# Kernel optimization log

Hardware: AMD Instinct MI355X
Metric: run time of the kernel (lower is better)

Reference implementation:

```python
import jax, jax.numpy as jnp
import numpy as np

B, L, D, NH, K, R = 2, 1024, 768, 12, 24, 768
HD = D // NH            # head_dim = 64
NFFT = 2048             # nearest power of two >= 2*L-1


def _spectral_filters():
    # Hankel matrix Z_{ij} = 2 / ((i+j)^3 - (i+j)), top-K eigvecs scaled by sigma^{1/4}
    e = np.arange(1, L + 1, dtype=np.float64)
    ipj = e[:, None] + e[None, :]
    Z = 2.0 / (ipj ** 3 - ipj)
    sigma, phi = np.linalg.eigh(Z)
    phi_k = phi[:, -K:] * (sigma[-K:] ** 0.25)
    return jnp.asarray(phi_k, dtype=jnp.float32)  # (L, K)


def setup_inputs() -> dict:
    key = jax.random.key(0)
    ks = jax.random.split(key, 16)
    s = 0.02
    lin = lambda k_, i, o: jax.random.normal(k_, (i, o), jnp.float32) * s
    return {
        "x": jax.random.normal(ks[0], (B, L, D), jnp.float32),
        "stu_filters": _spectral_filters(),
        "M_inputs": jax.random.normal(ks[1], (D, R), jnp.float32) * s,
        "M_filters": jax.random.normal(ks[2], (K, R), jnp.float32) * s,
        "wq_w": lin(ks[3], D, D), "wq_b": jnp.zeros((D,), jnp.float32),
        "wk_w": lin(ks[4], D, D), "wk_b": jnp.zeros((D,), jnp.float32),
        "wv_w": lin(ks[5], D, D), "wv_b": jnp.zeros((D,), jnp.float32),
        "wg_w": lin(ks[6], D, D), "wg_b": jnp.zeros((D,), jnp.float32),
        "wo_w": lin(ks[7], D, D), "wo_b": jnp.zeros((D,), jnp.float32),
    }


def _stu_features(x, stu_filters, M_inputs, M_filters):
    # tensordot STU path: project inputs and filters to rank R, then FFT causal conv
    u = x @ M_inputs                       # (B, L, R)
    phi = stu_filters @ M_filters          # (L, R)
    sgn = jnp.where(jnp.arange(L) % 2 == 0, 1.0, -1.0)[None, :, None]  # (1, L, 1)
    V = jnp.fft.rfft(phi, n=NFFT, axis=0)  # (NFFT//2+1, R)
    U = jnp.stack([u, u * sgn], axis=-1)   # (B, L, R, 2)
    Uf = jnp.fft.rfft(U, n=NFFT, axis=1)   # (B, NFFT//2+1, R, 2)
    conv = jnp.fft.irfft(V[None, :, :, None] * Uf, n=NFFT, axis=1)[:, :L]  # (B, L, R, 2)
    u_plus = conv[..., 0]
    u_minus = conv[..., 1] * sgn
    return u_plus + u_minus               # (B, L, R) with R == D


def reference(x, stu_filters, M_inputs, M_filters,
              wq_w, wq_b, wk_w, wk_b, wv_w, wv_b,
              wg_w, wg_b, wo_w, wo_b):
    x_tilde = _stu_features(x, stu_filters, M_inputs, M_filters)  # (B, L, D)

    heads = lambda y: y.reshape(B, L, NH, HD).transpose(0, 2, 1, 3)  # (B, H, L, h)
    q = heads(x @ wq_w + wq_b)
    k = heads(x @ wk_w + wk_b)
    v = heads(x @ wv_w + wv_b)

    # causal linear attention via cumulative outer-product state
    Z = jnp.einsum('bhtp,bhtn->bhtpn', v, k)     # (B, H, L, h, h)
    Hc = jnp.cumsum(Z, axis=2)
    Y = jnp.einsum('bhtp,bhtpn->bhtn', q, Hc)    # (B, H, L, h)
    y_attn = Y.transpose(0, 2, 1, 3).reshape(B, L, D)

    gate = jax.nn.sigmoid(x @ wg_w + wg_b)
    y = x_tilde + (y_attn - x_tilde) * gate
    return y @ wo_w + wo_b
```

## Files before the change

### kernel.cpp

```cpp
#include <hip/hip_runtime.h>
#include <math.h>

#define B_  2
#define L_  1024
#define D_  768
#define NH_ 12
#define HD_ 64
#define K_  24
#define R_  768
#define NC_ 16
#define CS_ 64

typedef __bf16 bf16x8 __attribute__((ext_vector_type(8)));
typedef float f32x4 __attribute__((ext_vector_type(4)));
typedef unsigned short u16x8 __attribute__((ext_vector_type(8)));

__device__ inline unsigned short f2bf(float f) {
    union { float f; unsigned u; } v; v.f = f;
    unsigned r = v.u + 0x7FFFu + ((v.u >> 16) & 1u);
    return (unsigned short)(r >> 16);
}

__device__ inline ushort4 pack4(const f32x4 v) {
    ushort4 r;
    r.x = f2bf(v[0]); r.y = f2bf(v[1]); r.z = f2bf(v[2]); r.w = f2bf(v[3]);
    return r;
}

#define GLD_LDS16(g, l)                                                     \
    __builtin_amdgcn_global_load_lds(                                       \
        (const __attribute__((address_space(1))) void*)(g),                 \
        (__attribute__((address_space(3))) void*)(l), 16, 0, 0)

__global__ __launch_bounds__(256) void k_prep(const float* __restrict__ w0,
                                              const float* __restrict__ w1,
                                              const float* __restrict__ w2,
                                              const float* __restrict__ w3,
                                              const float* __restrict__ w4,
                                              const float* __restrict__ w5,
                                              unsigned short* __restrict__ Wt,
                                              const float* __restrict__ x,
                                              unsigned short* __restrict__ xb,
                                              const float* __restrict__ F,
                                              const float* __restrict__ Mf,
                                              float* __restrict__ phi2) {
    const int bid = blockIdx.x;
    const int tid = threadIdx.x;
    if (bid < 864) {
        const int z = bid / 144, rem = bid % 144;
        const float* W;
        switch (z) {
            case 0: W = w0; break;
            case 1: W = w1; break;
            case 2: W = w2; break;
            case 3: W = w3; break;
            case 4: W = w4; break;
            default: W = w5; break;
        }
        unsigned short* o = Wt + (size_t)z * D_ * D_;
        __shared__ float t[64][65];
        const int n0 = (rem % 12) * 64, k0 = (rem / 12) * 64;
        const int c = tid & 63, rq = tid >> 6;
#pragma unroll
        for (int i = 0; i < 16; ++i)
            t[rq + i * 4][c] = W[(size_t)(k0 + rq + i * 4) * D_ + n0 + c];
        __syncthreads();
#pragma unroll
        for (int i = 0; i < 16; ++i)
            o[(size_t)(n0 + rq + i * 4) * D_ + k0 + c] = f2bf(t[c][rq + i * 4]);
    } else if (bid < 1632) {
        const int i8 = ((bid - 864) * 256 + tid) * 8;
        float4 f0 = *reinterpret_cast<const float4*>(x + i8);
        float4 f1 = *reinterpret_cast<const float4*>(x + i8 + 4);
        u16x8 p;
        p[0] = f2bf(f0.x); p[1] = f2bf(f0.y); p[2] = f2bf(f0.z); p[3] = f2bf(f0.w);
        p[4] = f2bf(f1.x); p[5] = f2bf(f1.y); p[6] = f2bf(f1.z); p[7] = f2bf(f1.w);
        *reinterpret_cast<u16x8*>(xb + i8) = p;
    } else {
        const int idx = (bid - 1632) * 256 + tid;
        const int r = idx % R_;
        const int j = idx / R_;
        float acc = 0.f;
#pragma unroll
        for (int kk = 0; kk < K_; ++kk)
            acc += F[j * K_ + kk] * Mf[kk * R_ + r];
        phi2[idx] = 2.f * acc;
    }
}

template <int FM, int FN>
__device__ __forceinline__ void gemm_core(const unsigned short* __restrict__ A,
                                          const unsigned short* __restrict__ Bt,
                                          const float* __restrict__ bias,
                                          int mode,
                                          float* __restrict__ cf,
                                          unsigned short* __restrict__ cbf,
                                          unsigned short* __restrict__ ct,
                                          int N, int Kd,
                                          int bm, int bn, int tid) {
    constexpr int BM = 2 * FM * 16;
    constexpr int BN = 2 * FN * 16;
    __shared__ unsigned short As[2][BM * 64];
    __shared__ unsigned short Bs[2][BN * 64];
    const int lane = tid & 63, wave = tid >> 6;
    const int wm = (wave >> 1) * (FM * 16), wn = (wave & 1) * (FN * 16);
    const int l15 = lane & 15, lg = lane >> 4;

    f32x4 acc[FM][FN] = {};

    auto stage = [&](int buf, int k0) {
#pragma unroll
        for (int q = 0; q < FM; ++q) {
            const int s = q * 256 + tid;
            GLD_LDS16(A + (size_t)(bm + (s >> 3)) * Kd + k0 + (s & 7) * 8,
                      &As[buf][s * 8]);
        }
#pragma unroll
        for (int q = 0; q < FN; ++q) {
            const int s = q * 256 + tid;
            GLD_LDS16(Bt + (size_t)(bn + (s >> 3)) * Kd + k0 + (s & 7) * 8,
                      &Bs[buf][s * 8]);
        }
    };

    stage(0, 0);
    __syncthreads();
    int cur = 0;
    const int nt = Kd / 64;
    for (int t = 0; t < nt; ++t) {
        if (t + 1 < nt) stage(cur ^ 1, (t + 1) * 64);
#pragma unroll
        for (int ks = 0; ks < 2; ++ks) {
            const int kb = ks * 32 + lg * 8;
            bf16x8 a[FM], b[FN];
#pragma unroll
            for (int f = 0; f < FM; ++f)
                a[f] = *reinterpret_cast<const bf16x8*>(
                    &As[cur][(wm + f * 16 + l15) * 64 + kb]);
#pragma unroll
            for (int f = 0; f < FN; ++f)
                b[f] = *reinterpret_cast<const bf16x8*>(
                    &Bs[cur][(wn + f * 16 + l15) * 64 + kb]);
#pragma unroll
            for (int fm = 0; fm < FM; ++fm)
#pragma unroll
                for (int fn = 0; fn < FN; ++fn)
                    acc[fm][fn] = __builtin_amdgcn_mfma_f32_16x16x32_bf16(
                        a[fm], b[fn], acc[fm][fn], 0, 0, 0);
        }
        __syncthreads();
        cur ^= 1;
    }

#pragma unroll
    for (int fm = 0; fm < FM; ++fm)
#pragma unroll
        for (int fn = 0; fn < FN; ++fn) {
            const int col = bn + wn + fn * 16 + l15;
            const float bv = bias ? bias[col] : 0.f;
            const int r0 = bm + wm + fm * 16 + lg * 4;
            f32x4 v = acc[fm][fn];
            v[0] += bv; v[1] += bv; v[2] += bv; v[3] += bv;
            if (mode == 0) {
#pragma unroll
                for (int j = 0; j < 4; ++j)
                    cf[(size_t)(r0 + j) * N + col] = v[j];
            }
            if (mode & 1) {
#pragma unroll
                for (int j = 0; j < 4; ++j)
                    cbf[(size_t)(r0 + j) * D_ + col] = f2bf(v[j]);
            }
            if (mode & 2) {
                const int h = col >> 6, n = col & 63;
                const int bI = r0 >> 10, l0 = r0 & 1023;
                *reinterpret_cast<ushort4*>(
                    ct + (((size_t)bI * NH_ + h) * 64 + n) * (size_t)L_ + l0) =
                    pack4(v);
            }
        }
}

__global__ __launch_bounds__(256) void k_gemm(const unsigned short* __restrict__ A,
                                              const unsigned short* __restrict__ Bt,
                                              const float* __restrict__ bias,
                                              float* __restrict__ C,
                                              int N, int Kd) {
    gemm_core<2, 2>(A, Bt, bias, 0, C, nullptr, nullptr, N, Kd,
                    blockIdx.y * 64, blockIdx.x * 64, threadIdx.x);
}

__global__ __launch_bounds__(256) void k_gemm5(const unsigned short* __restrict__ A,
                                               const unsigned short* __restrict__ wt,
                                               const float* __restrict__ bq,
                                               const float* __restrict__ bk,
                                               const float* __restrict__ bv,
                                               const float* __restrict__ bg,
                                               float* __restrict__ ubuf,
                                               unsigned short* __restrict__ qbf,
                                               unsigned short* __restrict__ ktb,
                                               unsigned short* __restrict__ vbf,
                                               unsigned short* __restrict__ vtb,
                                               float* __restrict__ gb) {
    const int z = blockIdx.z;
    const float* bias = nullptr;
    int mode = 0;
    float* cf = nullptr; unsigned short* cbf = nullptr; unsigned short* ct = nullptr;
    switch (z) {
        case 0: mode = 0; cf = ubuf; bias = nullptr; break;
        case 1: mode = 1; cbf = qbf; bias = bq; break;
        case 2: mode = 2; ct = ktb; bias = bk; break;
        case 3: mode = 3; cbf = vbf; ct = vtb; bias = bv; break;
        default: mode = 0; cf = gb; bias = bg; break;
    }
    const unsigned short* Bt = wt + (size_t)z * D_ * D_;
    gemm_core<4, 4>(A, Bt, bias, mode, cf, cbf, ct, D_, D_,
                    blockIdx.y * 128, blockIdx.x * 128, threadIdx.x);
}

__global__ __launch_bounds__(768) void k_conv(const float* __restrict__ u,
                                              const float* __restrict__ phi2,
                                              float* __restrict__ xt) {
    __shared__ f32x4 red[4][8][192];
    const int tid = threadIdx.x;
    const int g   = tid / 192;
    const int lr  = tid % 192;
    const int r   = lr * 4;
    const int m0  = blockIdx.x * 8;
    const int bp  = blockIdx.y;
    const int b   = bp >> 1, p = bp & 1;

    f32x4 acc[8] = {};
    f32x4 w[8]   = {};

    const int ns = g * 128;
    const int ne = min(ns + 128, m0 + 8);

    if (ns < ne) {
        if (g > 0) {
#pragma unroll
            for (int j = 1; j <= 7; ++j)
                w[(8 - j) & 7] =
                    *reinterpret_cast<const f32x4*>(phi2 + (size_t)(2 * (ns - j)) * R_ + r);
        }
        const float* pp = phi2 + (size_t)(2 * ns) * R_ + r;
        const float* up = u + ((size_t)(b * L_) + (size_t)(2 * (m0 + 7 - ns) + p)) * R_ + r;
        for (int i = ns; i < ne; i += 8) {
#pragma unroll
            for (int k = 0; k < 8; ++k) {
                const f32x4 wn = *reinterpret_cast<const f32x4*>(pp);
                const f32x4 un = *reinterpret_cast<const f32x4*>(up);
                w[k] = wn;
#pragma unroll
                for (int a = 0; a < 8; ++a)
                    acc[a] += w[(k + a + 1) & 7] * un;
                pp += 2 * R_;
                up -= 2 * R_;
            }
        }
    }

#pragma unroll
    for (int a = 0; a < 8; ++a) red[g][a][lr] = acc[a];
    __syncthreads();

#pragma unroll
    for (int q2 = 0; q2 < 2; ++q2) {
        const int sl = q2 * 768 + tid;
        const int a  = sl / 192, l = sl % 192;
        const f32x4 s = red[0][a][l] + red[1][a][l] + red[2][a][l] + red[3][a][l];
        *reinterpret_cast<f32x4*>(
            xt + ((size_t)(b * L_) + (size_t)(2 * (m0 + a) + p)) * R_ + l * 4) = s;
    }
}

__global__ __launch_bounds__(256) void k_attn(const unsigned short* __restrict__ qbf,
                                              const unsigned short* __restrict__ vbf,
                                              const unsigned short* __restrict__ ktb,
                                              const unsigned short* __restrict__ vtb,
                                              const float* __restrict__ xt,
                                              const float* __restrict__ g,
                                              unsigned short* __restrict__ gx) {
    const int c = blockIdx.x, h = blockIdx.y, b = blockIdx.z;
    __shared__ unsigned short Qs[64 * 64];
    __shared__ unsigned short Vs[64 * 64];
    __shared__ unsigned short Kc[64 * 64];
    __shared__ unsigned short Tk[64 * 64];
    __shared__ unsigned short Tv[64 * 64];
    __shared__ unsigned short Sl[64 * 72];
    __shared__ unsigned short Hl[64 * 72];

    const int tid = threadIdx.x;
    const int lane = tid & 63, wave = tid >> 6;
    const int wr = (wave >> 1) * 32, wc = (wave & 1) * 32;
    const int l15 = lane & 15, lg = lane >> 4;

    {
        const size_t rowbase = ((size_t)(b * L_ + c * CS_)) * D_ + h * HD_;
        const size_t tbase = ((size_t)(b * NH_ + h)) * 64 * (size_t)L_ + c * 64;
#pragma unroll
        for (int q2 = 0; q2 < 2; ++q2) {
            const int s = q2 * 256 + tid;
            const int row = s >> 3, c8 = s & 7;
            GLD_LDS16(qbf + rowbase + (size_t)row * D_ + c8 * 8, &Qs[s * 8]);
            GLD_LDS16(vbf + rowbase + (size_t)row * D_ + c8 * 8, &Vs[s * 8]);
            GLD_LDS16(ktb + tbase + (size_t)row * L_ + c8 * 8, &Kc[s * 8]);
        }
    }

    f32x4 hacc[2][2] = {};
    for (int cc = 0; cc < c; ++cc) {
        __syncthreads();
        const size_t tb2 = ((size_t)(b * NH_ + h)) * 64 * (size_t)L_ + cc * 64;
#pragma unroll
        for (int q2 = 0; q2 < 2; ++q2) {
            const int s = q2 * 256 + tid;
            const int row = s >> 3, c8 = s & 7;
            GLD_LDS16(ktb + tb2 + (size_t)row * L_ + c8 * 8, &Tk[s * 8]);
            GLD_LDS16(vtb + tb2 + (size_t)row * L_ + c8 * 8, &Tv[s * 8]);
        }
        __syncthreads();
#pragma unroll
        for (int ks = 0; ks < 2; ++ks) {
            const int kb = ks * 32 + lg * 8;
            bf16x8 av[2], bk[2];
#pragma unroll
            for (int f = 0; f < 2; ++f) {
                av[f] = *reinterpret_cast<const bf16x8*>(&Tv[(wr + f * 16 + l15) * 64 + kb]);
                bk[f] = *reinterpret_cast<const bf16x8*>(&Tk[(wc + f * 16 + l15) * 64 + kb]);
            }
#pragma unroll
            for (int fm = 0; fm < 2; ++fm)
#pragma unroll
                for (int fn = 0; fn < 2; ++fn)
                    hacc[fm][fn] = __builtin_amdgcn_mfma_f32_16x16x32_bf16(
                        av[fm], bk[fn], hacc[fm][fn], 0, 0, 0);
        }
    }
    __syncthreads();

    if (c > 0) {
#pragma unroll
        for (int fm = 0; fm < 2; ++fm)
#pragma unroll
            for (int fn = 0; fn < 2; ++fn) {
                const int n = wc + fn * 16 + l15;
                const int p0 = wr + fm * 16 + lg * 4;
                *reinterpret_cast<ushort4*>(&Hl[n * 72 + p0]) = pack4(hacc[fm][fn]);
            }
    }

    {
        f32x4 sacc[2][2] = {};
#pragma unroll
        for (int ks = 0; ks < 2; ++ks) {
            const int kb = ks * 32 + lg * 8;
            bf16x8 av[2], bq[2];
#pragma unroll
            for (int f = 0; f < 2; ++f) {
                av[f] = *reinterpret_cast<const bf16x8*>(&Vs[(wr + f * 16 + l15) * 64 + kb]);
                bq[f] = *reinterpret_cast<const bf16x8*>(&Qs[(wc + f * 16 + l15) * 64 + kb]);
            }
#pragma unroll
            for (int fm = 0; fm < 2; ++fm)
#pragma unroll
                for (int fn = 0; fn < 2; ++fn)
                    sacc[fm][fn] = __builtin_amdgcn_mfma_f32_16x16x32_bf16(
                        av[fm], bq[fn], sacc[fm][fn], 0, 0, 0);
        }
#pragma unroll
        for (int fm = 0; fm < 2; ++fm)
#pragma unroll
            for (int fn = 0; fn < 2; ++fn) {
                const int t = wc + fn * 16 + l15;
                const int s0 = wr + fm * 16 + lg * 4;
#pragma unroll
                for (int j = 0; j < 4; ++j)
                    if (s0 + j > t) sacc[fm][fn][j] = 0.f;
                *reinterpret_cast<ushort4*>(&Sl[t * 72 + s0]) = pack4(sacc[fm][fn]);
            }
    }
    __syncthreads();

    f32x4 yacc[2][2] = {};
#pragma unroll
    for (int ks = 0; ks < 2; ++ks) {
        const int kb = ks * 32 + lg * 8;
        bf16x8 ak[2], bs[2];
#pragma unroll
        for (int f = 0; f < 2; ++f) {
            ak[f] = *reinterpret_cast<const bf16x8*>(&Kc[(wr + f * 16 + l15) * 64 + kb]);
            bs[f] = *reinterpret_cast<const bf16x8*>(&Sl[(wc + f * 16 + l15) * 72 + kb]);
        }
#pragma unroll
        for (int fm = 0; fm < 2; ++fm)
#pragma unroll
            for (int fn = 0; fn < 2; ++fn)
                yacc[fm][fn] = __builtin_amdgcn_mfma_f32_16x16x32_bf16(
                    ak[fm], bs[fn], yacc[fm][fn], 0, 0, 0);
    }
    if (c > 0) {
#pragma unroll
        for (int ks = 0; ks < 2; ++ks) {
            const int kb = ks * 32 + lg * 8;
            bf16x8 ah[2], bq[2];
#pragma unroll
            for (int f = 0; f < 2; ++f) {
                ah[f] = *reinterpret_cast<const bf16x8*>(&Hl[(wr + f * 16 + l15) * 72 + kb]);
                bq[f] = *reinterpret_cast<const bf16x8*>(&Qs[(wc + f * 16 + l15) * 64 + kb]);
            }
#pragma unroll
            for (int fm = 0; fm < 2; ++fm)
#pragma unroll
                for (int fn = 0; fn < 2; ++fn)
                    yacc[fm][fn] = __builtin_amdgcn_mfma_f32_16x16x32_bf16(
                        ah[fm], bq[fn], yacc[fm][fn], 0, 0, 0);
        }
    }

#pragma unroll
    for (int fm = 0; fm < 2; ++fm)
#pragma unroll
        for (int fn = 0; fn < 2; ++fn) {
            const int n0 = wr + fm * 16 + lg * 4;
            const int t = wc + fn * 16 + l15;
            const size_t idx = ((size_t)(b * L_ + c * CS_ + t)) * D_ + h * HD_ + n0;
            const float4 gv = *reinterpret_cast<const float4*>(g + idx);
            const float4 xv = *reinterpret_cast<const float4*>(xt + idx);
            f32x4 y = yacc[fm][fn];
            ushort4 o;
            {
                const float s0 = 1.f / (1.f + expf(-gv.x));
                o.x = f2bf(xv.x + (y[0] - xv.x) * s0);
                const float s1 = 1.f / (1.f + expf(-gv.y));
                o.y = f2bf(xv.y + (y[1] - xv.y) * s1);
                const float s2 = 1.f / (1.f + expf(-gv.z));
                o.z = f2bf(xv.z + (y[2] - xv.z) * s2);
                const float s3 = 1.f / (1.f + expf(-gv.w));
                o.w = f2bf(xv.w + (y[3] - xv.w) * s3);
            }
            *reinterpret_cast<ushort4*>(gx + idx) = o;
        }
}

extern "C" void kernel_launch(void* const* d_in, const int* in_sizes, int n_in,
                              void* d_out, int out_size, void* d_ws, size_t ws_size,
                              hipStream_t stream) {
    const float* x    = (const float*)d_in[0];
    const float* stu  = (const float*)d_in[1];
    const float* Mi   = (const float*)d_in[2];
    const float* Mf   = (const float*)d_in[3];
    const float* wq_w = (const float*)d_in[4];
    const float* wq_b = (const float*)d_in[5];
    const float* wk_w = (const float*)d_in[6];
    const float* wk_b = (const float*)d_in[7];
    const float* wv_w = (const float*)d_in[8];
    const float* wv_b = (const float*)d_in[9];
    const float* wg_w = (const float*)d_in[10];
    const float* wg_b = (const float*)d_in[11];
    const float* wo_w = (const float*)d_in[12];
    const float* wo_b = (const float*)d_in[13];
    float* out = (float*)d_out;

    char* ws = (char*)d_ws;
    size_t o = 0;
    const size_t WSZ = (size_t)D_ * D_;
    unsigned short* wbf = (unsigned short*)(ws + o); o += 6 * WSZ * 2;
    unsigned short* xbf = (unsigned short*)(ws + o); o += (size_t)B_ * L_ * D_ * 2;
    unsigned short* gx  = (unsigned short*)(ws + o); o += (size_t)B_ * L_ * D_ * 2;
    unsigned short* qbf = (unsigned short*)(ws + o); o += (size_t)B_ * L_ * D_ * 2;
    unsigned short* vbf = (unsigned short*)(ws + o); o += (size_t)B_ * L_ * D_ * 2;
    unsigned short* ktb = (unsigned short*)(ws + o); o += (size_t)B_ * NH_ * 64 * L_ * 2;
    unsigned short* vtb = (unsigned short*)(ws + o); o += (size_t)B_ * NH_ * 64 * L_ * 2;
    float* ubuf = (float*)(ws + o); o += (size_t)B_ * L_ * R_ * 4;
    float* phi2 = (float*)(ws + o); o += (size_t)L_ * R_ * 4;
    float* xt   = (float*)(ws + o); o += (size_t)B_ * L_ * R_ * 4;
    float* gb   = (float*)(ws + o); o += (size_t)B_ * L_ * D_ * 4;

    unsigned short* wo_t = wbf + 5 * WSZ;

    const dim3 blk(256);

    k_prep<<<dim3(4704), blk, 0, stream>>>(Mi, wq_w, wk_w, wv_w, wg_w, wo_w, wbf,
                                           x, xbf, stu, Mf, phi2);

    k_gemm5<<<dim3(D_ / 128, (B_ * L_) / 128, 5), blk, 0, stream>>>(
        xbf, wbf, wq_b, wk_b, wv_b, wg_b, ubuf, qbf, ktb, vbf, vtb, gb);

    k_conv<<<dim3(L_ / 2 / 8, B_ * 2), dim3(768), 0, stream>>>(ubuf, phi2, xt);

    k_attn<<<dim3(NC_, NH_, B_), blk, 0, stream>>>(qbf, vbf, ktb, vtb, xt, gb, gx);

    k_gemm<<<dim3(D_ / 64, (B_ * L_) / 64), blk, 0, stream>>>(gx, wo_t, wo_b, out, D_, D_);
}
```

Before: 100.0 us.

## Store conv operands in bf16, compute only even filter taps, move gating into conv

The u and gate projections and the filter table are now stored as bf16 instead of fp32. Only the even-index filter rows are precomputed, since the conv only ever reads those, which halves the phi table and shrinks the prep grid. The gating blend moves from the attention kernel into the convolution kernel, which now runs after attention and reads a bf16 attention output. The conv reduction uses 8 groups of 64 taps with 8-wide vectors, and its cross-group partial sums are stored in bf16 in LDS, which risks extra precision loss in both operands and accumulation.

```diff
diff --git a/kernel.cpp b/kernel.cpp
--- a/kernel.cpp
+++ b/kernel.cpp
@@ -13,6 +13,7 @@
 
 typedef __bf16 bf16x8 __attribute__((ext_vector_type(8)));
 typedef float f32x4 __attribute__((ext_vector_type(4)));
+typedef float f32x8 __attribute__((ext_vector_type(8)));
 typedef unsigned short u16x8 __attribute__((ext_vector_type(8)));
 
 __device__ inline unsigned short f2bf(float f) {
@@ -24,6 +25,24 @@
 __device__ inline ushort4 pack4(const f32x4 v) {
     ushort4 r;
     r.x = f2bf(v[0]); r.y = f2bf(v[1]); r.z = f2bf(v[2]); r.w = f2bf(v[3]);
+    return r;
+}
+
+__device__ inline u16x8 pack8(const f32x8 v) {
+    u16x8 r;
+#pragma unroll
+    for (int e = 0; e < 8; ++e) r[e] = f2bf(v[e]);
+    return r;
+}
+
+__device__ inline f32x8 bf2f8(const u16x8 v) {
+    f32x8 r;
+#pragma unroll
+    for (int e = 0; e < 8; ++e) {
+        union { float f; unsigned u; } t;
+        t.u = ((unsigned)v[e]) << 16;
+        r[e] = t.f;
+    }
     return r;
 }
 
@@ -43,7 +62,7 @@
                                               unsigned short* __restrict__ xb,
                                               const float* __restrict__ F,
                                               const float* __restrict__ Mf,
-                                              float* __restrict__ phi2) {
+                                              unsigned short* __restrict__ phiev) {
     const int bid = blockIdx.x;
     const int tid = threadIdx.x;
     if (bid < 864) {
@@ -79,12 +98,12 @@
     } else {
         const int idx = (bid - 1632) * 256 + tid;
         const int r = idx % R_;
-        const int j = idx / R_;
+        const int n = idx / R_;
         float acc = 0.f;
 #pragma unroll
         for (int kk = 0; kk < K_; ++kk)
-            acc += F[j * K_ + kk] * Mf[kk * R_ + r];
-        phi2[idx] = 2.f * acc;
+            acc += F[(2 * n) * K_ + kk] * Mf[kk * R_ + r];
+        phiev[idx] = f2bf(2.f * acc);
     }
 }
 
@@ -196,91 +215,33 @@
                                                const float* __restrict__ bk,
                                                const float* __restrict__ bv,
                                                const float* __restrict__ bg,
-                                               float* __restrict__ ubuf,
+                                               unsigned short* __restrict__ ubf,
                                                unsigned short* __restrict__ qbf,
                                                unsigned short* __restrict__ ktb,
                                                unsigned short* __restrict__ vbf,
                                                unsigned short* __restrict__ vtb,
-                                               float* __restrict__ gb) {
+                                               unsigned short* __restrict__ gbf) {
     const int z = blockIdx.z;
     const float* bias = nullptr;
-    int mode = 0;
-    float* cf = nullptr; unsigned short* cbf = nullptr; unsigned short* ct = nullptr;
+    int mode = 1;
+    unsigned short* cbf = nullptr; unsigned short* ct = nullptr;
     switch (z) {
-        case 0: mode = 0; cf = ubuf; bias = nullptr; break;
+        case 0: mode = 1; cbf = ubf; bias = nullptr; break;
         case 1: mode = 1; cbf = qbf; bias = bq; break;
         case 2: mode = 2; ct = ktb; bias = bk; break;
         case 3: mode = 3; cbf = vbf; ct = vtb; bias = bv; break;
-        default: mode = 0; cf = gb; bias = bg; break;
+        default: mode = 1; cbf = gbf; bias = bg; break;
     }
     const unsigned short* Bt = wt + (size_t)z * D_ * D_;
-    gemm_core<4, 4>(A, Bt, bias, mode, cf, cbf, ct, D_, D_,
+    gemm_core<4, 4>(A, Bt, bias, mode, nullptr, cbf, ct, D_, D_,
                     blockIdx.y * 128, blockIdx.x * 128, threadIdx.x);
-}
-
-__global__ __launch_bounds__(768) void k_conv(const float* __restrict__ u,
-                                              const float* __restrict__ phi2,
-                                              float* __restrict__ xt) {
-    __shared__ f32x4 red[4][8][192];
-    const int tid = threadIdx.x;
-    const int g   = tid / 192;
-    const int lr  = tid % 192;
-    const int r   = lr * 4;
-    const int m0  = blockIdx.x * 8;
-    const int bp  = blockIdx.y;
-    const int b   = bp >> 1, p = bp & 1;
-
-    f32x4 acc[8] = {};
-    f32x4 w[8]   = {};
-
-    const int ns = g * 128;
-    const int ne = min(ns + 128, m0 + 8);
-
-    if (ns < ne) {
-        if (g > 0) {
-#pragma unroll
-            for (int j = 1; j <= 7; ++j)
-                w[(8 - j) & 7] =
-                    *reinterpret_cast<const f32x4*>(phi2 + (size_t)(2 * (ns - j)) * R_ + r);
-        }
-        const float* pp = phi2 + (size_t)(2 * ns) * R_ + r;
-        const float* up = u + ((size_t)(b * L_) + (size_t)(2 * (m0 + 7 - ns) + p)) * R_ + r;
-        for (int i = ns; i < ne; i += 8) {
-#pragma unroll
-            for (int k = 0; k < 8; ++k) {
-                const f32x4 wn = *reinterpret_cast<const f32x4*>(pp);
-                const f32x4 un = *reinterpret_cast<const f32x4*>(up);
-                w[k] = wn;
-#pragma unroll
-                for (int a = 0; a < 8; ++a)
-                    acc[a] += w[(k + a + 1) & 7] * un;
-                pp += 2 * R_;
-                up -= 2 * R_;
-            }
-        }
-    }
-
-#pragma unroll
-    for (int a = 0; a < 8; ++a) red[g][a][lr] = acc[a];
-    __syncthreads();
-
-#pragma unroll
-    for (int q2 = 0; q2 < 2; ++q2) {
-        const int sl = q2 * 768 + tid;
-        const int a  = sl / 192, l = sl % 192;
-        const f32x4 s = red[0][a][l] + red[1][a][l] + red[2][a][l] + red[3][a][l];
-        *reinterpret_cast<f32x4*>(
-            xt + ((size_t)(b * L_) + (size_t)(2 * (m0 + a) + p)) * R_ + l * 4) = s;
-    }
 }
 
 __global__ __launch_bounds__(256) void k_attn(const unsigned short* __restrict__ qbf,
                                               const unsigned short* __restrict__ vbf,
                                               const unsigned short* __restrict__ ktb,
                                               const unsigned short* __restrict__ vtb,
-                                              const float* __restrict__ xt,
-                                              const float* __restrict__ g,
-                                              unsigned short* __restrict__ gx) {
+                                              unsigned short* __restrict__ yab) {
     const int c = blockIdx.x, h = blockIdx.y, b = blockIdx.z;
     __shared__ unsigned short Qs[64 * 64];
     __shared__ unsigned short Vs[64 * 64];
@@ -425,22 +386,75 @@
             const int n0 = wr + fm * 16 + lg * 4;
             const int t = wc + fn * 16 + l15;
             const size_t idx = ((size_t)(b * L_ + c * CS_ + t)) * D_ + h * HD_ + n0;
-            const float4 gv = *reinterpret_cast<const float4*>(g + idx);
-            const float4 xv = *reinterpret_cast<const float4*>(xt + idx);
-            f32x4 y = yacc[fm][fn];
-            ushort4 o;
-            {
-                const float s0 = 1.f / (1.f + expf(-gv.x));
-                o.x = f2bf(xv.x + (y[0] - xv.x) * s0);
-                const float s1 = 1.f / (1.f + expf(-gv.y));
-                o.y = f2bf(xv.y + (y[1] - xv.y) * s1);
-                const float s2 = 1.f / (1.f + expf(-gv.z));
-                o.z = f2bf(xv.z + (y[2] - xv.z) * s2);
-                const float s3 = 1.f / (1.f + expf(-gv.w));
-                o.w = f2bf(xv.w + (y[3] - xv.w) * s3);
-            }
-            *reinterpret_cast<ushort4*>(gx + idx) = o;
-        }
+            *reinterpret_cast<ushort4*>(yab + idx) = pack4(yacc[fm][fn]);
+        }
+}
+
+__global__ __launch_bounds__(768) void k_conv(const unsigned short* __restrict__ ubf,
+                                              const unsigned short* __restrict__ phiev,
+                                              const unsigned short* __restrict__ yab,
+                                              const unsigned short* __restrict__ gbf,
+                                              unsigned short* __restrict__ gx) {
+    __shared__ u16x8 red[8][8][96];
+    const int tid = threadIdx.x;
+    const int g   = tid / 96;
+    const int lr  = tid % 96;
+    const int r   = lr * 8;
+    const int m0  = blockIdx.x * 8;
+    const int bp  = blockIdx.y;
+    const int b   = bp >> 1, p = bp & 1;
+
+    f32x8 acc[8] = {};
+    f32x8 w[8]   = {};
+
+    const int ns = g * 64;
+    const int ne = min(ns + 64, m0 + 8);
+
+    if (ns < ne) {
+        if (g > 0) {
+#pragma unroll
+            for (int j = 1; j <= 7; ++j)
+                w[(8 - j) & 7] = bf2f8(
+                    *reinterpret_cast<const u16x8*>(phiev + (size_t)(ns - j) * R_ + r));
+        }
+        const unsigned short* pp = phiev + (size_t)ns * R_ + r;
+        const unsigned short* up =
+            ubf + ((size_t)(b * L_) + (size_t)(2 * (m0 + 7 - ns) + p)) * R_ + r;
+        for (int i = ns; i < ne; i += 8) {
+#pragma unroll
+            for (int k = 0; k < 8; ++k) {
+                const u16x8 pv = *reinterpret_cast<const u16x8*>(pp);
+                const u16x8 uv = *reinterpret_cast<const u16x8*>(up);
+                w[k] = bf2f8(pv);
+                const f32x8 fu = bf2f8(uv);
+#pragma unroll
+                for (int a = 0; a < 8; ++a)
+                    acc[a] += w[(k + a + 1) & 7] * fu;
+                pp += R_;
+                up -= 2 * R_;
+            }
+        }
+    }
+
+#pragma unroll
+    for (int a = 0; a < 8; ++a) red[g][a][lr] = pack8(acc[a]);
+    __syncthreads();
+
+    const int a2 = tid / 96, l2 = tid % 96;
+    f32x8 s = {};
+#pragma unroll
+    for (int g2 = 0; g2 < 8; ++g2) s += bf2f8(red[g2][a2][l2]);
+
+    const size_t idx = ((size_t)(b * L_) + (size_t)(2 * (m0 + a2) + p)) * R_ + l2 * 8;
+    const f32x8 yf = bf2f8(*reinterpret_cast<const u16x8*>(yab + idx));
+    const f32x8 gf = bf2f8(*reinterpret_cast<const u16x8*>(gbf + idx));
+    u16x8 o;
+#pragma unroll
+    for (int e = 0; e < 8; ++e) {
+        const float sg = 1.f / (1.f + expf(-gf[e]));
+        o[e] = f2bf(s[e] + (yf[e] - s[e]) * sg);
+    }
+    *reinterpret_cast<u16x8*>(gx + idx) = o;
 }
 
 extern "C" void kernel_launch(void* const* d_in, const int* in_sizes, int n_in,
@@ -465,31 +479,31 @@
     char* ws = (char*)d_ws;
     size_t o = 0;
     const size_t WSZ = (size_t)D_ * D_;
-    unsigned short* wbf = (unsigned short*)(ws + o); o += 6 * WSZ * 2;
-    unsigned short* xbf = (unsigned short*)(ws + o); o += (size_t)B_ * L_ * D_ * 2;
-    unsigned short* gx  = (unsigned short*)(ws + o); o += (size_t)B_ * L_ * D_ * 2;
-    unsigned short* qbf = (unsigned short*)(ws + o); o += (size_t)B_ * L_ * D_ * 2;
-    unsigned short* vbf = (unsigned short*)(ws + o); o += (size_t)B_ * L_ * D_ * 2;
-    unsigned short* ktb = (unsigned short*)(ws + o); o += (size_t)B_ * NH_ * 64 * L_ * 2;
-    unsigned short* vtb = (unsigned short*)(ws + o); o += (size_t)B_ * NH_ * 64 * L_ * 2;
-    float* ubuf = (float*)(ws + o); o += (size_t)B_ * L_ * R_ * 4;
-    float* phi2 = (float*)(ws + o); o += (size_t)L_ * R_ * 4;
-    float* xt   = (float*)(ws + o); o += (size_t)B_ * L_ * R_ * 4;
-    float* gb   = (float*)(ws + o); o += (size_t)B_ * L_ * D_ * 4;
+    unsigned short* wbf   = (unsigned short*)(ws + o); o += 6 * WSZ * 2;
+    unsigned short* xbf   = (unsigned short*)(ws + o); o += (size_t)B_ * L_ * D_ * 2;
+    unsigned short* gx    = (unsigned short*)(ws + o); o += (size_t)B_ * L_ * D_ * 2;
+    unsigned short* qbf   = (unsigned short*)(ws + o); o += (size_t)B_ * L_ * D_ * 2;
+    unsigned short* vbf   = (unsigned short*)(ws + o); o += (size_t)B_ * L_ * D_ * 2;
+    unsigned short* ubf   = (unsigned short*)(ws + o); o += (size_t)B_ * L_ * D_ * 2;
+    unsigned short* gbf   = (unsigned short*)(ws + o); o += (size_t)B_ * L_ * D_ * 2;
+    unsigned short* yab   = (unsigned short*)(ws + o); o += (size_t)B_ * L_ * D_ * 2;
+    unsigned short* ktb   = (unsigned short*)(ws + o); o += (size_t)B_ * NH_ * 64 * L_ * 2;
+    unsigned short* vtb   = (unsigned short*)(ws + o); o += (size_t)B_ * NH_ * 64 * L_ * 2;
+    unsigned short* phiev = (unsigned short*)(ws + o); o += (size_t)(L_ / 2) * R_ * 2;
 
     unsigned short* wo_t = wbf + 5 * WSZ;
 
     const dim3 blk(256);
 
-    k_prep<<<dim3(4704), blk, 0, stream>>>(Mi, wq_w, wk_w, wv_w, wg_w, wo_w, wbf,
-                                           x, xbf, stu, Mf, phi2);
+    k_prep<<<dim3(3168), blk, 0, stream>>>(Mi, wq_w, wk_w, wv_w, wg_w, wo_w, wbf,
+                                           x, xbf, stu, Mf, phiev);
 
     k_gemm5<<<dim3(D_ / 128, (B_ * L_) / 128, 5), blk, 0, stream>>>(
-        xbf, wbf, wq_b, wk_b, wv_b, wg_b, ubuf, qbf, ktb, vbf, vtb, gb);
-
-    k_conv<<<dim3(L_ / 2 / 8, B_ * 2), dim3(768), 0, stream>>>(ubuf, phi2, xt);
-
-    k_attn<<<dim3(NC_, NH_, B_), blk, 0, stream>>>(qbf, vbf, ktb, vtb, xt, gb, gx);
+        xbf, wbf, wq_b, wk_b, wv_b, wg_b, ubf, qbf, ktb, vbf, vtb, gbf);
+
+    k_attn<<<dim3(NC_, NH_, B_), blk, 0, stream>>>(qbf, vbf, ktb, vtb, yab);
+
+    k_conv<<<dim3(L_ / 2 / 8, B_ * 2), dim3(768), 0, stream>>>(ubf, phiev, yab, gbf, gx);
 
     k_gemm<<<dim3(D_ / 64, (B_ * L_) / 64), blk, 0, stream>>>(gx, wo_t, wo_b, out, D_, D_);
 }
```

New measurement: 96.04 us. 4.0% less time.
